# Kernel optimization log

Measured on AMD Instinct MI355X. Metric: run time of the kernel, lower is better.

Reference implementation:

```python
import jax, jax.numpy as jnp
import numpy as np

B, L, NW, E, H = 64, 128, 30000, 300, 256
NE, NA = 34, 36  # num_events, num_arguments


def setup_inputs() -> dict:
    key = jax.random.key(0)
    ks = jax.random.split(key, 12)
    init = lambda k, sh: jax.random.normal(k, sh, dtype=jnp.float32) * 0.05
    return {
        "input_ids": jax.random.randint(ks[0], (B, L), 0, NW),
        "emb_table": init(ks[1], (NW, E)),
        "w_ih_f": init(ks[2], (4 * H, E)),
        "w_hh_f": init(ks[3], (4 * H, H)),
        "b_f": init(ks[4], (4 * H,)),
        "w_ih_b": init(ks[5], (4 * H, E)),
        "w_hh_b": init(ks[6], (4 * H, H)),
        "b_b": init(ks[7], (4 * H,)),
        "event_w": init(ks[8], (NE, 2 * H)),
        "event_b": init(ks[9], (NE,)),
        "arg_w": init(ks[10], (NA, 4 * H + (NA - 1) + (NE - 1))),
        "b_dummy": None,
        "arg_b": init(ks[11], (NA,)),
    } if False else {
        "input_ids": jax.random.randint(ks[0], (B, L), 0, NW),
        "emb_table": init(ks[1], (NW, E)),
        "w_ih_f": init(ks[2], (4 * H, E)),
        "w_hh_f": init(ks[3], (4 * H, H)),
        "b_f": init(ks[4], (4 * H,)),
        "w_ih_b": init(ks[5], (4 * H, E)),
        "w_hh_b": init(ks[6], (4 * H, H)),
        "b_b": init(ks[7], (4 * H,)),
        "event_w": init(ks[8], (NE, 2 * H)),
        "event_b": init(ks[9], (NE,)),
        "arg_w": init(ks[10], (NA, 4 * H + (NA - 1) + (NE - 1))),
        "arg_b": init(ks[11], (NA,)),
    }


def _lstm_dir(x, w_ih, w_hh, b, reverse):
    # x: [B, L, E] -> hidden states [B, L, H] (PyTorch gate order i,f,g,o; b = b_ih + b_hh)
    Bx = x.shape[0]
    Hh = w_hh.shape[1]
    xg = jnp.einsum("ble,ge->blg", x, w_ih) + b  # [B, L, 4H]

    def step(carry, xt):
        h, c = carry
        g = xt + h @ w_hh.T
        i, f, gg, o = jnp.split(g, 4, axis=-1)
        c = jax.nn.sigmoid(f) * c + jax.nn.sigmoid(i) * jnp.tanh(gg)
        h = jax.nn.sigmoid(o) * jnp.tanh(c)
        return (h, c), h

    init = (jnp.zeros((Bx, Hh), x.dtype), jnp.zeros((Bx, Hh), x.dtype))
    _, hs = jax.lax.scan(step, init, jnp.swapaxes(xg, 0, 1), reverse=reverse)
    return jnp.swapaxes(hs, 0, 1)


def _forward(input_ids, emb_table, w_ih_f, w_hh_f, b_f, w_ih_b, w_hh_b, b_b,
             event_w, event_b, arg_w, arg_b):
    emb = emb_table[input_ids]  # [B, L, E]
    hf = _lstm_dir(emb, w_ih_f, w_hh_f, b_f, False)
    hb = _lstm_dir(emb, w_ih_b, w_hh_b, b_b, True)
    hs = jnp.concatenate([hf, hb], axis=-1)  # [B, L, 2H]
    Bx = hs.shape[0]
    g_trg_arg0 = jnp.zeros((Bx, L, NE - 1), hs.dtype)
    g_arg0 = jnp.zeros((Bx, L, NA - 1), hs.dtype)

    def step(carry, trig_h):  # trig_h: [B, 2H] = hidden_states[:, i]
        g_trg_arg, g_arg = carry
        ev_logit = trig_h @ event_w.T + event_b          # [B, NE]
        ev_pred = jnp.argmax(ev_logit, axis=-1)          # [B]
        trig_rep = jnp.broadcast_to(trig_h[:, None, :], hs.shape)
        feat = jnp.concatenate([hs, trig_rep, g_arg, g_trg_arg], axis=-1)
        arg_logits = feat @ arg_w.T + arg_b              # [B, L, NA]
        arg_pred = jnp.argmax(arg_logits, axis=-1)       # [B, L]
        active = (ev_pred > 0)[:, None, None]            # batch has a trigger
        pos = (arg_pred > 0)[:, :, None]                 # positions with an argument
        # update_g_trg_arg: set column (ev_pred-1) to 1 where argument predicted
        ev_oh = jax.nn.one_hot(ev_pred - 1, NE - 1, dtype=bool)[:, None, :]
        g_trg_arg = jnp.where(active & pos & ev_oh, jnp.asarray(1.0, g_trg_arg.dtype), g_trg_arg)
        # update_g_arg: set g_arg[b, j, arg_pred-1] = 1 where arg_pred>0 and active
        arg_oh = jax.nn.one_hot(arg_pred - 1, NA - 1, dtype=bool)
        g_arg = jnp.where(active & pos & arg_oh, jnp.asarray(1.0, g_arg.dtype), g_arg)
        return (g_trg_arg, g_arg), (ev_logit, arg_logits)

    _, (ev_logits, arg_logits) = jax.lax.scan(step, (g_trg_arg0, g_arg0), jnp.swapaxes(hs, 0, 1))
    return jnp.swapaxes(ev_logits, 0, 1), jnp.swapaxes(arg_logits, 0, 1)


def reference(input_ids, emb_table, w_ih_f, w_hh_f, b_f, w_ih_b, w_hh_b, b_b,
              event_w, event_b, arg_w, arg_b):
    return _forward(input_ids, emb_table, w_ih_f, w_hh_f, b_f, w_ih_b, w_hh_b, b_b,
                    event_w, event_b, arg_w, arg_b)
```

## Files before the change

### kernel.cpp

```cpp
#include <hip/hip_runtime.h>
#include <hip/hip_bf16.h>
#include <cstring>

typedef __attribute__((ext_vector_type(4))) float floatx4;
typedef unsigned int u32;
typedef unsigned short u16;

#define DEV static __device__ __forceinline__
DEV float sigf(float x){ return 1.f / (1.f + expf(-x)); }


__global__ __launch_bounds__(256) void k_pack_whh(const float* __restrict__ whf,
                                                  const float* __restrict__ whb,
                                                  float* __restrict__ wP)
{
  int i = blockIdx.x * 256 + threadIdx.x;
  if (i >= 524288) return;
  int dir = i >> 18, rem = i & 262143, g = rem >> 8, k = rem & 255;
  const float v = (dir ? whb : whf)[g*256 + k];
  wP[(size_t)(k >> 2)*8192 + (size_t)(dir*1024 + g)*4 + (k & 3)] = v;
}

__global__ __launch_bounds__(256) void k_pack_wcat(const float* __restrict__ evw,
                                                   const float* __restrict__ argw,
                                                   float* __restrict__ WcatT)
{
  int i = blockIdx.x * 256 + threadIdx.x;
  if (i >= 65536) return;
  int k = i >> 7, col = i & 127;
  float v = 0.f;
  if (col < 34)        v = evw[(size_t)col*512 + k];
  else if (col < 70)   v = argw[(size_t)(col-34)*1092 + 512 + k];
  else if (col < 106)  v = argw[(size_t)(col-70)*1092 + k];
  WcatT[(size_t)k*128 + col] = v;
}

__global__ __launch_bounds__(256) void k_xg(const int* __restrict__ ids,
    const float* __restrict__ emb,
    const float* __restrict__ wihf, const float* __restrict__ wihb,
    const float* __restrict__ bf_, const float* __restrict__ bb_,
    float* __restrict__ xg)
{
  const int dir = blockIdx.z;
  const float* W    = dir ? wihb : wihf;
  const float* bias = dir ? bb_  : bf_;
  const int n0 = blockIdx.x * 64, m0 = blockIdx.y * 64;
  __shared__ float As[16][64];
  __shared__ float Bs[16][64];
  const int tid = threadIdx.x;
  const int row = tid & 63, kk = (tid >> 6) * 4;
  const int tx = tid & 15, ty = tid >> 4;
  const size_t abase = (size_t)ids[m0 + row] * 300;
  const size_t bbase = (size_t)(n0 + row) * 300;
  float acc[4][4] = {};

  for (int k0 = 0; k0 < 300; k0 += 16) {
    __syncthreads();
    {
      const int gk = k0 + kk;
      floatx4 va = {0,0,0,0}, vb = {0,0,0,0};
      if (gk + 3 < 300) {
        va = *(const floatx4*)(emb + abase + gk);
        vb = *(const floatx4*)(W   + bbase + gk);
      } else {
        #pragma unroll
        for (int j = 0; j < 4; j++) if (gk + j < 300) {
          va[j] = emb[abase + gk + j];
          vb[j] = W[bbase + gk + j];
        }
      }
      #pragma unroll
      for (int j = 0; j < 4; j++){ As[kk+j][row] = va[j]; Bs[kk+j][row] = vb[j]; }
    }
    __syncthreads();
    #pragma unroll
    for (int k = 0; k < 16; k++){
      const floatx4 av = *(const floatx4*)&As[k][ty*4];
      const floatx4 bv = *(const floatx4*)&Bs[k][tx*4];
      #pragma unroll
      for (int i = 0; i < 4; i++)
        #pragma unroll
        for (int j = 0; j < 4; j++) acc[i][j] += av[i] * bv[j];
    }
  }
  const floatx4 bv = *(const floatx4*)(bias + n0 + tx*4);
  #pragma unroll
  for (int i = 0; i < 4; i++){
    const int m = m0 + ty*4 + i;
    floatx4 o;
    #pragma unroll
    for (int j = 0; j < 4; j++) o[j] = acc[i][j] + bv[j];
    *(floatx4*)&xg[(size_t)dir*8388608 + (size_t)m*1024 + n0 + tx*4] = o;
  }
}

__global__ __launch_bounds__(1024) void k_lstm(const float* __restrict__ xg,
    const float* __restrict__ wP, float* __restrict__ hs)
{
  const int wg = blockIdx.x;
  const int dir = wg >> 6, b = wg & 63, dirbase = dir * 1024;
  const int t = threadIdx.x;
  __shared__ float __align__(16) hl[2][256];
  __shared__ float gates[1024];

  const float* wp  = wP + (size_t)(dirbase + t) * 4;
  const float* xg0 = xg + (size_t)dir*8388608 + (size_t)b*131072;

  float c = 0.f;
  if (t < 256) hl[0][t] = 0.f;
  __syncthreads();

  for (int s = 0; s < 128; s++){
    const int tstep = dir ? (127 - s) : s;
    const float x0 = __builtin_nontemporal_load(xg0 + (size_t)tstep*1024 + t);
    const float* h0 = hl[s & 1];
    float a0 = 0.f;

    #pragma unroll 8
    for (int q = 0; q < 64; q++){
      const floatx4 wv = *(const floatx4*)(wp + (size_t)q*8192);
      const floatx4 hv = *(const floatx4*)&h0[q*4];
      #pragma unroll
      for (int e = 0; e < 4; e++) a0 += wv[e] * hv[e];
    }

    gates[t] = x0 + a0;
    __syncthreads();
    if (t < 256){
      const float gi = gates[t],       gf = gates[256 + t],
                  gg = gates[512 + t], go = gates[768 + t];
      c = sigf(gf)*c + sigf(gi)*tanhf(gg);
      const float h = sigf(go)*tanhf(c);
      hl[(s + 1) & 1][t] = h;
      hs[(size_t)b*65536 + (size_t)tstep*512 + dir*256 + t] = h;
    }
    __syncthreads();
  }
}

__global__ __launch_bounds__(256) void k_hmm(const float* __restrict__ hs,
    const float* __restrict__ WcatT, float* __restrict__ P)
{
  const int n0 = blockIdx.x * 64, m0 = blockIdx.y * 64;
  __shared__ float As[16][64];
  __shared__ float Bs[16][64];
  const int tid = threadIdx.x;
  const int row = tid & 63, kk = (tid >> 6) * 4;
  const int tx = tid & 15, ty = tid >> 4;
  float acc[4][4] = {};

  for (int k0 = 0; k0 < 512; k0 += 16) {
    __syncthreads();
    {
      const floatx4 va = *(const floatx4*)(hs + (size_t)(m0+row)*512 + k0 + kk);
      #pragma unroll
      for (int j = 0; j < 4; j++){
        As[kk+j][row] = va[j];
        Bs[kk+j][row] = WcatT[(size_t)(k0+kk+j)*128 + n0 + row];
      }
    }
    __syncthreads();
    #pragma unroll
    for (int k = 0; k < 16; k++){
      const floatx4 av = *(const floatx4*)&As[k][ty*4];
      const floatx4 bv = *(const floatx4*)&Bs[k][tx*4];
      #pragma unroll
      for (int i = 0; i < 4; i++)
        #pragma unroll
        for (int j = 0; j < 4; j++) acc[i][j] += av[i] * bv[j];
    }
  }
  #pragma unroll
  for (int i = 0; i < 4; i++){
    floatx4 o;
    #pragma unroll
    for (int j = 0; j < 4; j++) o[j] = acc[i][j];
    *(floatx4*)&P[(size_t)(m0 + ty*4 + i)*128 + n0 + tx*4] = o;
  }
}

__global__ __launch_bounds__(256) void k_post(const float* __restrict__ P,
    const float* __restrict__ evb, const float* __restrict__ argb,
    float* __restrict__ ev_out, float* __restrict__ trig,
    float* __restrict__ base, int* __restrict__ evact)
{
  const int m = blockIdx.x * 256 + threadIdx.x;
  const float* row = P + (size_t)m*128;
  float bestv = row[0] + evb[0]; int besti = 0;
  ev_out[(size_t)m*34] = bestv;
  for (int n = 1; n < 34; n++){
    const float v = row[n] + evb[n];
    ev_out[(size_t)m*34 + n] = v;
    if (v > bestv){ bestv = v; besti = n; }
  }
  evact[m] = besti;
  for (int n = 0; n < 36; n++) trig[(size_t)m*36 + n] = row[34 + n];
  for (int n = 0; n < 36; n++) base[(size_t)m*36 + n] = row[70 + n] + argb[n];
}

__global__ __launch_bounds__(128) void k_dec(const float* __restrict__ trig,
    const float* __restrict__ base, const int* __restrict__ evact,
    const float* __restrict__ arg_w, float* __restrict__ out1)
{
  const int bb = blockIdx.x >> 1, jh = blockIdx.x & 1;
  const int tid = threadIdx.x;
  const int j = jh*64 + (tid >> 1), p = tid & 1;
  __shared__ float trig_l[128*36];
  __shared__ float Wg_l[35*36];
  __shared__ float Wtg_l[33*36];
  __shared__ int evact_l[128];

  for (int f = tid; f < 128*36; f += 128) trig_l[f] = trig[(size_t)bb*4608 + f];
  for (int f = tid; f < 35*36; f += 128){ int k = f/36, a = f - k*36; Wg_l[f]  = arg_w[(size_t)a*1092 + 1024 + k]; }
  for (int f = tid; f < 33*36; f += 128){ int k = f/36, a = f - k*36; Wtg_l[f] = arg_w[(size_t)a*1092 + 1059 + k]; }
  evact_l[tid] = evact[bb*128 + tid];

  float basev[18], contrib[18];
  #pragma unroll
  for (int x = 0; x < 18; x++){
    basev[x] = base[((size_t)bb*128 + j)*36 + p*18 + x];
    contrib[x] = 0.f;
  }
  unsigned long long garg = 0ull, gtrg = 0ull;
  __syncthreads();

  float* outb = out1 + (size_t)bb*589824 + (size_t)j*36;

  for (int i = 0; i < 128; i++){
    const float* tr = &trig_l[i*36 + p*18];
    float l[18];
    #pragma unroll
    for (int x = 0; x < 18; x++) l[x] = basev[x] + contrib[x] + tr[x];
    float mv = l[0]; int mi = p*18;
    #pragma unroll
    for (int x = 1; x < 18; x++){ if (l[x] > mv){ mv = l[x]; mi = p*18 + x; } }
    const float ov = __shfl_xor(mv, 1);
    const int   oi = __shfl_xor(mi, 1);
    const float v0 = p ? ov : mv, v1 = p ? mv : ov;
    const int   i0 = p ? oi : mi, i1 = p ? mi : oi;
    const int gidx = (v1 > v0) ? i1 : i0;

    float* po = outb + (size_t)i*4608 + p*18;
    #pragma unroll
    for (int x = 0; x < 18; x++) po[x] = l[x];

    const int ev = evact_l[i];
    if (ev > 0 && gidx > 0){
      const int k1 = gidx - 1;
      const unsigned long long bit1 = 1ull << k1;
      if (!(garg & bit1)){
        garg |= bit1;
        const float* wc = &Wg_l[k1*36 + p*18];
        #pragma unroll
        for (int x = 0; x < 18; x++) contrib[x] += wc[x];
      }
      const int k2 = ev - 1;
      const unsigned long long bit2 = 1ull << k2;
      if (!(gtrg & bit2)){
        gtrg |= bit2;
        const float* wc = &Wtg_l[k2*36 + p*18];
        #pragma unroll
        for (int x = 0; x < 18; x++) contrib[x] += wc[x];
      }
    }
  }
}

extern "C" void kernel_launch(void* const* d_in, const int* in_sizes, int n_in,
                              void* d_out, int out_size, void* d_ws, size_t ws_size,
                              hipStream_t stream)
{
  const int*   ids  = (const int*)d_in[0];
  const float* emb  = (const float*)d_in[1];
  const float* wihf = (const float*)d_in[2];
  const float* whhf = (const float*)d_in[3];
  const float* bf_  = (const float*)d_in[4];
  const float* wihb = (const float*)d_in[5];
  const float* whhb = (const float*)d_in[6];
  const float* bb_  = (const float*)d_in[7];
  const float* evw  = (const float*)d_in[8];
  const float* evb  = (const float*)d_in[9];
  const float* argw = (const float*)d_in[10];
  const float* argb = (const float*)d_in[11];

  char* ws = (char*)d_ws;
  float* xg    = (float*)(ws + 0);
  float* wP    = (float*)(ws + 67108864);
  float* WcatT = (float*)(ws + 69206016);
  float* hs    = (float*)(ws + 69468160);
  float* P     = (float*)(ws + 86245376);
  float* trig  = (float*)(ws + 90439680);
  float* base  = (float*)(ws + 91619328);
  int*   evact = (int*)  (ws + 92798976);

  float* ev_out  = (float*)d_out;
  float* arg_out = ev_out + 278528;

  k_pack_whh <<<2048, 256, 0, stream>>>(whhf, whhb, wP);
  k_pack_wcat<<<256, 256, 0, stream>>>(evw, argw, WcatT);
  k_xg  <<<dim3(16, 128, 2), 256, 0, stream>>>(ids, emb, wihf, wihb, bf_, bb_, xg);
  k_lstm<<<128, 1024, 0, stream>>>(xg, wP, hs);
  k_hmm <<<dim3(2, 128), 256, 0, stream>>>(hs, WcatT, P);
  k_post<<<32, 256, 0, stream>>>(P, evb, argb, ev_out, trig, base, evact);
  k_dec <<<128, 128, 0, stream>>>(trig, base, evact, argw, arg_out);
}
```

Baseline: 1.409 ms.

## Split LSTM recurrence across four workgroups with register-resident weights and atomic sync

The recurrent LSTM kernel now gives each (direction, batch) sequence to four 256-thread workgroups instead of one 1024-thread workgroup. Each workgroup owns one gate block. Each thread keeps its row of W_hh in registers (48 float4) plus LDS (16 float4), so the weights are no longer re-read from global memory every timestep, and the packing kernel is removed. At each step the four workgroups exchange gate pre-activations through a global buffer and synchronise with release/acquire sequence counters. This adds inter-workgroup latency per step and relies on all 512 workgroups being co-resident to avoid deadlock.

Result: slower. 3.685 ms (+161.5%).

```diff
diff --git a/kernel.cpp b/kernel.cpp
--- a/kernel.cpp
+++ b/kernel.cpp
@@ -10,15 +10,9 @@
 DEV float sigf(float x){ return 1.f / (1.f + expf(-x)); }
 
 
-__global__ __launch_bounds__(256) void k_pack_whh(const float* __restrict__ whf,
-                                                  const float* __restrict__ whb,
-                                                  float* __restrict__ wP)
-{
-  int i = blockIdx.x * 256 + threadIdx.x;
-  if (i >= 524288) return;
-  int dir = i >> 18, rem = i & 262143, g = rem >> 8, k = rem & 255;
-  const float v = (dir ? whb : whf)[g*256 + k];
-  wP[(size_t)(k >> 2)*8192 + (size_t)(dir*1024 + g)*4 + (k & 3)] = v;
+__global__ __launch_bounds__(256) void k_zero(u32* __restrict__ p)
+{
+  p[blockIdx.x * 256 + threadIdx.x] = 0u;
 }
 
 __global__ __launch_bounds__(256) void k_pack_wcat(const float* __restrict__ evw,
@@ -94,46 +88,79 @@
   }
 }
 
-__global__ __launch_bounds__(1024) void k_lstm(const float* __restrict__ xg,
-    const float* __restrict__ wP, float* __restrict__ hs)
-{
-  const int wg = blockIdx.x;
-  const int dir = wg >> 6, b = wg & 63, dirbase = dir * 1024;
+__global__ __launch_bounds__(256) void k_lstm(const float* __restrict__ xg,
+    const float* __restrict__ whhf, const float* __restrict__ whhb,
+    float* __restrict__ hglob, float* __restrict__ gbuf,
+    u32* __restrict__ seq, float* __restrict__ hs)
+{
+  const int wgid = blockIdx.x;
+  const int grp = wgid >> 2, gt = wgid & 3;
+  const int dir = grp >> 6, b = grp & 63;
   const int t = threadIdx.x;
-  __shared__ float __align__(16) hl[2][256];
-  __shared__ float gates[1024];
-
-  const float* wp  = wP + (size_t)(dirbase + t) * 4;
-  const float* xg0 = xg + (size_t)dir*8388608 + (size_t)b*131072;
-
+  const int g = gt*256 + t;
+
+  __shared__ floatx4 wl[16][256];
+
+  const float* wrow = (dir ? whhb : whhf) + (size_t)g * 256;
+  floatx4 w4[48];
+  #pragma unroll
+  for (int q = 0; q < 48; q++) w4[q] = *(const floatx4*)(wrow + q*4);
+  #pragma unroll
+  for (int q = 0; q < 16; q++) wl[q][t] = *(const floatx4*)(wrow + 192 + q*4);
+
+  float* hb = hglob + (size_t)wgid * 256;
+  hb[t] = 0.f;
   float c = 0.f;
-  if (t < 256) hl[0][t] = 0.f;
+
+  const float* xgbase = xg + (size_t)dir*8388608 + (size_t)b*131072;
+  float* gslotbase = gbuf + (size_t)grp*2048;
+  u32*   seqbase   = seq  + (size_t)grp*8;
   __syncthreads();
 
   for (int s = 0; s < 128; s++){
     const int tstep = dir ? (127 - s) : s;
-    const float x0 = __builtin_nontemporal_load(xg0 + (size_t)tstep*1024 + t);
-    const float* h0 = hl[s & 1];
-    float a0 = 0.f;
-
-    #pragma unroll 8
-    for (int q = 0; q < 64; q++){
-      const floatx4 wv = *(const floatx4*)(wp + (size_t)q*8192);
-      const floatx4 hv = *(const floatx4*)&h0[q*4];
-      #pragma unroll
-      for (int e = 0; e < 4; e++) a0 += wv[e] * hv[e];
-    }
-
-    gates[t] = x0 + a0;
-    __syncthreads();
-    if (t < 256){
-      const float gi = gates[t],       gf = gates[256 + t],
-                  gg = gates[512 + t], go = gates[768 + t];
-      c = sigf(gf)*c + sigf(gi)*tanhf(gg);
-      const float h = sigf(go)*tanhf(c);
-      hl[(s + 1) & 1][t] = h;
-      hs[(size_t)b*65536 + (size_t)tstep*512 + dir*256 + t] = h;
-    }
+    const int par = s & 1;
+    const float x0 = __builtin_nontemporal_load(xgbase + (size_t)tstep*1024 + g);
+
+    float a = 0.f;
+    #pragma unroll
+    for (int q = 0; q < 48; q++){
+      const floatx4 hv = *(const floatx4*)(hb + q*4);
+      a += w4[q][0]*hv[0]; a += w4[q][1]*hv[1];
+      a += w4[q][2]*hv[2]; a += w4[q][3]*hv[3];
+    }
+    #pragma unroll
+    for (int q = 0; q < 16; q++){
+      const floatx4 hv = *(const floatx4*)(hb + 192 + q*4);
+      const floatx4 wv = wl[q][t];
+      a += wv[0]*hv[0]; a += wv[1]*hv[1];
+      a += wv[2]*hv[2]; a += wv[3]*hv[3];
+    }
+    a += x0;
+
+    float* gslot = gslotbase + par*1024 + gt*256;
+    gslot[t] = a;
+    __syncthreads();
+    u32* sq = seqbase + par*4;
+    if (t == 0){
+      __hip_atomic_store(&sq[gt], (u32)(s + 1), __ATOMIC_RELEASE, __HIP_MEMORY_SCOPE_AGENT);
+      const int o1 = (gt+1)&3, o2 = (gt+2)&3, o3 = (gt+3)&3;
+      while (__hip_atomic_load(&sq[o1], __ATOMIC_ACQUIRE, __HIP_MEMORY_SCOPE_AGENT) < (u32)(s+1)) {}
+      while (__hip_atomic_load(&sq[o2], __ATOMIC_ACQUIRE, __HIP_MEMORY_SCOPE_AGENT) < (u32)(s+1)) {}
+      while (__hip_atomic_load(&sq[o3], __ATOMIC_ACQUIRE, __HIP_MEMORY_SCOPE_AGENT) < (u32)(s+1)) {}
+    }
+    __syncthreads();
+
+    float* gp = gslotbase + par*1024;
+    const float vi = (gt==0) ? a : __hip_atomic_load(gp +       t, __ATOMIC_RELAXED, __HIP_MEMORY_SCOPE_AGENT);
+    const float vf = (gt==1) ? a : __hip_atomic_load(gp + 256 + t, __ATOMIC_RELAXED, __HIP_MEMORY_SCOPE_AGENT);
+    const float vg = (gt==2) ? a : __hip_atomic_load(gp + 512 + t, __ATOMIC_RELAXED, __HIP_MEMORY_SCOPE_AGENT);
+    const float vo = (gt==3) ? a : __hip_atomic_load(gp + 768 + t, __ATOMIC_RELAXED, __HIP_MEMORY_SCOPE_AGENT);
+
+    c = sigf(vf)*c + sigf(vi)*tanhf(vg);
+    const float h = sigf(vo)*tanhf(c);
+    hb[t] = h;
+    if (gt == 3) hs[(size_t)b*65536 + (size_t)tstep*512 + dir*256 + t] = h;
     __syncthreads();
   }
 }
@@ -285,7 +312,9 @@
 
   char* ws = (char*)d_ws;
   float* xg    = (float*)(ws + 0);
-  float* wP    = (float*)(ws + 67108864);
+  float* hglob = (float*)(ws + 67108864);
+  float* gbuf  = (float*)(ws + 67633152);
+  u32*   seq   = (u32*)  (ws + 68681728);
   float* WcatT = (float*)(ws + 69206016);
   float* hs    = (float*)(ws + 69468160);
   float* P     = (float*)(ws + 86245376);
@@ -296,10 +325,10 @@
   float* ev_out  = (float*)d_out;
   float* arg_out = ev_out + 278528;
 
-  k_pack_whh <<<2048, 256, 0, stream>>>(whhf, whhb, wP);
+  k_zero     <<<4, 256, 0, stream>>>(seq);
   k_pack_wcat<<<256, 256, 0, stream>>>(evw, argw, WcatT);
   k_xg  <<<dim3(16, 128, 2), 256, 0, stream>>>(ids, emb, wihf, wihb, bf_, bb_, xg);
-  k_lstm<<<128, 1024, 0, stream>>>(xg, wP, hs);
+  k_lstm<<<512, 256, 0, stream>>>(xg, whhf, whhb, hglob, gbuf, seq, hs);
   k_hmm <<<dim3(2, 128), 256, 0, stream>>>(hs, WcatT, P);
   k_post<<<32, 256, 0, stream>>>(P, evb, argb, ev_out, trig, base, evact);
   k_dec <<<128, 128, 0, stream>>>(trig, base, evact, argw, arg_out);
```
